# Kernel optimization log

Hardware: AMD Instinct MI355X
Metric: run time of the kernel (lower is better)

Reference implementation:

```python
import jax, jax.numpy as jnp
import numpy as np

B, G, NPA, NT, L = 8192, 689, 16, 131, 6
S = G + NPA * NT  # 2785 = 689 genes + 16 nodes per each of 131 assemblies


def setup_inputs() -> dict:
    key = jax.random.key(0)
    ks = jax.random.split(key, 8)
    x = jax.random.normal(ks[0], (B, G), dtype=jnp.float32)
    # depth-0 mask: place the 689 gene inputs into the first 689 slots of the layer
    lm0 = jnp.zeros((G, S), jnp.float32).at[jnp.arange(G), jnp.arange(G)].set(1.0)
    # per-depth sparse binary connectivity masks (ontology DAG edges at each depth)
    lm = (jax.random.uniform(ks[1], (L, S, S)) < 0.02).astype(jnp.float32)
    # diagonal pass-through masks for edges skipping this depth (stored as diagonals)
    flm_diag = (jax.random.uniform(ks[2], (L, S)) < 0.3).astype(jnp.float32)
    # final assembly selector: the nodes_per_assembly slots of the root assembly
    fasm = jnp.zeros((S,), jnp.float32).at[G:G + NPA].set(1.0)
    W0 = jax.random.normal(ks[3], (G, S), dtype=jnp.float32) * 0.05
    b0 = jnp.zeros((S,), jnp.float32)
    W = jax.random.normal(ks[4], (L, S, S), dtype=jnp.float32) * 0.05
    b = jnp.zeros((L, S), jnp.float32)
    gamma = jnp.ones((L + 1, S), jnp.float32)
    beta = jnp.zeros((L + 1, S), jnp.float32)
    w_out = jax.random.normal(ks[5], (S,), dtype=jnp.float32) * 0.05
    b_out = jnp.zeros((), jnp.float32)
    return {"x": x, "lm0": lm0, "lm": lm, "flm_diag": flm_diag, "fasm": fasm,
            "W0": W0, "b0": b0, "W": W, "b": b, "gamma": gamma, "beta": beta,
            "w_out": w_out, "b_out": b_out}


def _bn(h, g, bt, eps=1e-5):
    # training-mode BatchNorm1d over the batch axis
    m = h.mean(axis=0)
    v = h.var(axis=0)
    return (h - m) * jax.lax.rsqrt(v + eps) * g + bt


def reference(x, lm0, lm, flm_diag, fasm, W0, b0, W, b, gamma, beta, w_out, b_out):
    # depth 0: masked linear placing genes into layer slots, BN before activation
    h = jnp.tanh(_bn(x @ (W0 * lm0) + b0, gamma[0], beta[0]))  # [B, S]
    def step(h, layer):
        Wl, bl, lml, dl, gl, btl = layer
        # masked linear + BN + activation, plus diagonal pass-through skip
        hn = jnp.tanh(_bn(h @ (Wl * lml) + bl, gl, btl)) + h * dl
        return hn, None
    h, _ = jax.lax.scan(step, h, (W, b, lm, flm_diag, gamma[1:], beta[1:]))
    # output_method='final': linear head on final-assembly nodes only
    return (h * fasm) @ w_out + b_out  # [B]
```

## Files before the change

### kernel.cpp

```cpp
#include <hip/hip_runtime.h>
#include <hip/hip_fp16.h>
#include <stdint.h>

typedef uint32_t u32;
typedef uint64_t u64;
typedef unsigned int v4u __attribute__((ext_vector_type(4)));
typedef float v4f __attribute__((ext_vector_type(4)));
typedef _Float16 v2h __attribute__((ext_vector_type(2)));

constexpr int CB   = 8192;
constexpr int CG   = 689;
constexpr int CL   = 6;
constexpr int CS   = 2785;
constexpr int CSP  = 2816;
constexpr int CRS  = 8256;
constexpr int KCAP = 112;

union V16 { v4u u; v2h h2[4]; };
union F4  { v4f v; float f[4]; u32 u[4]; };
union HW  { u32 u; v2h h; };

__global__ __launch_bounds__(256) void build_main(const float* __restrict__ lm,
                                                  const float* __restrict__ W,
                                                  u64* __restrict__ ent,
                                                  int* __restrict__ cnt)
{
    int rb = blockIdx.x;
    int l  = rb / CS;
    int j  = rb - l * CS;
    const float* lrow = lm + (size_t)rb * CS;
    const float* wrow = W  + (size_t)rb * CS;
    u64 hi = ((u64)((u32)j * (u32)(CRS * 2))) << 32;
    int colbase = l * CSP;

    for (int s4 = threadIdx.x * 4; s4 < CS; s4 += 1024) {
        if (s4 + 4 <= CS) {
            F4 m4; m4.v = *reinterpret_cast<const v4f*>(lrow + s4);
            if ((m4.u[0] | m4.u[1] | m4.u[2] | m4.u[3]) == 0u) continue;
            F4 w4; w4.v = *reinterpret_cast<const v4f*>(wrow + s4);
#pragma unroll
            for (int q = 0; q < 4; q++) {
                if (m4.f[q] != 0.0f) {
                    int s = s4 + q;
                    int pos = atomicAdd(&cnt[colbase + s], 1);
                    if (pos < KCAP) {
                        u32 hw = (u32)__half_as_ushort(__float2half(w4.f[q]));
                        ent[(size_t)(colbase + s) * KCAP + pos] = hi | (u64)(hw | (hw << 16));
                    }
                }
            }
        } else {
            for (int s = s4; s < CS; s++) {
                float m = lrow[s];
                if (m != 0.0f) {
                    int pos = atomicAdd(&cnt[colbase + s], 1);
                    if (pos < KCAP) {
                        u32 hw = (u32)__half_as_ushort(__float2half(wrow[s]));
                        ent[(size_t)(colbase + s) * KCAP + pos] = hi | (u64)(hw | (hw << 16));
                    }
                }
            }
        }
    }
}

__global__ __launch_bounds__(256) void build0(const float* __restrict__ lm0,
                                              const float* __restrict__ W0,
                                              u64* __restrict__ ent,
                                              int* __restrict__ cnt)
{
    int j = blockIdx.x;
    const float* lrow = lm0 + (size_t)j * CS;
    const float* wrow = W0  + (size_t)j * CS;
    u64 hi = ((u64)((u32)j * (u32)(CRS * 2))) << 32;
    for (int s4 = threadIdx.x * 4; s4 < CS; s4 += 1024) {
        if (s4 + 4 <= CS) {
            F4 m4; m4.v = *reinterpret_cast<const v4f*>(lrow + s4);
            if ((m4.u[0] | m4.u[1] | m4.u[2] | m4.u[3]) == 0u) continue;
            F4 w4; w4.v = *reinterpret_cast<const v4f*>(wrow + s4);
#pragma unroll
            for (int q = 0; q < 4; q++) {
                if (m4.f[q] != 0.0f) {
                    int s = s4 + q;
                    int pos = atomicAdd(&cnt[s], 1);
                    if (pos < KCAP) {
                        u32 hw = (u32)__half_as_ushort(__float2half(w4.f[q]));
                        ent[(size_t)s * KCAP + pos] = hi | (u64)(hw | (hw << 16));
                    }
                }
            }
        } else {
            for (int s = s4; s < CS; s++) {
                float m = lrow[s];
                if (m != 0.0f) {
                    int pos = atomicAdd(&cnt[s], 1);
                    if (pos < KCAP) {
                        u32 hw = (u32)__half_as_ushort(__float2half(wrow[s]));
                        ent[(size_t)s * KCAP + pos] = hi | (u64)(hw | (hw << 16));
                    }
                }
            }
        }
    }
}

__global__ __launch_bounds__(256) void transpose_x(const float* __restrict__ x,
                                                   __half* __restrict__ xT)
{
    __shared__ float tile[32][33];
    int gx = blockIdx.x * 32;
    int gy = blockIdx.y * 32;
    int tx = threadIdx.x, ty = threadIdx.y;
#pragma unroll
    for (int i = 0; i < 32; i += 8) {
        int g = gx + tx;
        int b = gy + ty + i;
        tile[ty + i][tx] = (g < CG) ? x[(size_t)b * CG + g] : 0.f;
    }
    __syncthreads();
#pragma unroll
    for (int i = 0; i < 32; i += 8) {
        int g = gx + ty + i;
        int b = gy + tx;
        if (g < CG) xT[(size_t)g * CRS + b] = __float2half(tile[tx][ty + i]);
    }
}

__global__ __launch_bounds__(64) void gather_k(const __half* __restrict__ src,
                                               __half* __restrict__ dst,
                                               const u64* __restrict__ ent,
                                               const int* __restrict__ cnt,
                                               const float* __restrict__ bias,
                                               float* __restrict__ sumv,
                                               float* __restrict__ sumq,
                                               const int* __restrict__ sel,
                                               const int* __restrict__ selcnt)
{
    int s;
    if (sel) {
        if ((int)blockIdx.y >= *selcnt) return;
        s = sel[blockIdx.y];
    } else {
        s = blockIdx.y;
    }
    int lane = threadIdx.x;
    int boff = blockIdx.z * 4096 + blockIdx.x * 512 + lane * 8;

    int n = cnt[s]; if (n > KCAP) n = KCAP;
    int ng = (n + 7) >> 3;
    const u64* e = ent + (size_t)s * KCAP;
    const char* sb = (const char*)src + (size_t)boff * 2;

    float bv = bias[s];
    float acc[8];
#pragma unroll
    for (int j = 0; j < 8; j++) acc[j] = bv;

    for (int g = 0; g < ng; g++) {
        u64 ev[8];
#pragma unroll
        for (int q = 0; q < 8; q++) ev[q] = e[g * 8 + q];
        V16 rv[8];
#pragma unroll
        for (int q = 0; q < 8; q++)
            rv[q].u = *reinterpret_cast<const v4u*>(sb + (u32)(ev[q] >> 32));
#pragma unroll
        for (int q = 0; q < 8; q++) {
            HW w2; w2.u = (u32)ev[q];
#pragma unroll
            for (int j = 0; j < 4; j++) {
                float2 a2;
                a2.x = acc[2*j]; a2.y = acc[2*j+1];
#if __has_builtin(__builtin_amdgcn_fdot2)
#endif
                (void)a2;
                float2 f = __half22float2(*(const __half2*)&rv[q].h2[j]);
                float w = __half2float(*(const __half*)&w2.h);
                acc[2*j]   = fmaf(w, f.x, acc[2*j]);
                acc[2*j+1] = fmaf(w, f.y, acc[2*j+1]);
            }
        }
    }

    V16 o;
#pragma unroll
    for (int j = 0; j < 4; j++) {
        v2h p; p.x = (_Float16)acc[2*j]; p.y = (_Float16)acc[2*j+1];
        o.h2[j] = p;
    }
    __builtin_nontemporal_store(o.u, reinterpret_cast<v4u*>(dst + (size_t)s * CRS + boff));

    float ls = 0.f, lq = 0.f;
#pragma unroll
    for (int j = 0; j < 8; j++) { ls += acc[j]; lq += acc[j] * acc[j]; }
#pragma unroll
    for (int off = 32; off > 0; off >>= 1) {
        ls += __shfl_xor(ls, off);
        lq += __shfl_xor(lq, off);
    }
    if (lane == 0) { atomicAdd(&sumv[s], ls); atomicAdd(&sumq[s], lq); }
}

__global__ __launch_bounds__(64) void bn_act(__half* __restrict__ h,
                                             const __half* __restrict__ prev,
                                             const float* __restrict__ sumv,
                                             const float* __restrict__ sumq,
                                             const float* __restrict__ gamma,
                                             const float* __restrict__ beta,
                                             const float* __restrict__ dlv)
{
    int s = blockIdx.y;
    int boff = blockIdx.x * 512 + threadIdx.x * 8;
    float mean = sumv[s] * (1.0f / CB);
    float var  = sumq[s] * (1.0f / CB) - mean * mean;
    float rstd = rsqrtf(var + 1e-5f);
    float scale = gamma[s] * rstd;
    float shift = beta[s] - mean * scale;
    size_t base = (size_t)s * CRS + boff;
    V16 v; v.u = *reinterpret_cast<const v4u*>(h + base);
    V16 pv;
    float d = 0.f;
    if (prev) { d = dlv[s]; pv.u = *reinterpret_cast<const v4u*>(prev + base); }
    V16 o;
#pragma unroll
    for (int j = 0; j < 4; j++) {
        float2 f = __half22float2(*(const __half2*)&v.h2[j]);
        float t0 = tanhf(fmaf(f.x, scale, shift));
        float t1 = tanhf(fmaf(f.y, scale, shift));
        if (prev) {
            float2 p = __half22float2(*(const __half2*)&pv.h2[j]);
            t0 = fmaf(d, p.x, t0);
            t1 = fmaf(d, p.y, t1);
        }
        v2h pk; pk.x = (_Float16)t0; pk.y = (_Float16)t1;
        o.h2[j] = pk;
    }
    *reinterpret_cast<v4u*>(h + base) = o.u;
}

__global__ __launch_bounds__(256) void head_prep(const float* __restrict__ fasm,
                                                 const float* __restrict__ wout,
                                                 int* __restrict__ hcnt,
                                                 int* __restrict__ hs,
                                                 float* __restrict__ hc)
{
    int s = blockIdx.x * 256 + threadIdx.x;
    if (s >= CS) return;
    float c = fasm[s] * wout[s];
    if (c != 0.f) {
        int p = atomicAdd(hcnt, 1);
        if (p < 64) { hs[p] = s; hc[p] = c; }
    }
}

__global__ __launch_bounds__(256) void head_k(const __half* __restrict__ h6pre,
                                              const __half* __restrict__ h5,
                                              const int* __restrict__ hcnt,
                                              const int* __restrict__ hs,
                                              const float* __restrict__ hc,
                                              const float* __restrict__ sumv,
                                              const float* __restrict__ sumq,
                                              const float* __restrict__ gamma,
                                              const float* __restrict__ beta,
                                              const float* __restrict__ dlv,
                                              const float* __restrict__ bout,
                                              float* __restrict__ out)
{
    int b = blockIdx.x * 256 + threadIdx.x;
    int n = *hcnt; if (n > 64) n = 64;
    float acc = bout[0];
    for (int k = 0; k < n; k++) {
        int s = hs[k];
        float mean = sumv[s] * (1.0f / CB);
        float var  = sumq[s] * (1.0f / CB) - mean * mean;
        float rstd = rsqrtf(var + 1e-5f);
        float scale = gamma[s] * rstd;
        float shift = beta[s] - mean * scale;
        float pre  = __half2float(h6pre[(size_t)s * CRS + b]);
        float prev = __half2float(h5[(size_t)s * CRS + b]);
        float hn = tanhf(fmaf(pre, scale, shift)) + dlv[s] * prev;
        acc = fmaf(hc[k], hn, acc);
    }
    out[b] = acc;
}

extern "C" void kernel_launch(void* const* d_in, const int* in_sizes, int n_in,
                              void* d_out, int out_size, void* d_ws, size_t ws_size,
                              hipStream_t stream)
{
    const float* x    = (const float*)d_in[0];
    const float* lm0  = (const float*)d_in[1];
    const float* lm   = (const float*)d_in[2];
    const float* flm  = (const float*)d_in[3];
    const float* fasm = (const float*)d_in[4];
    const float* W0   = (const float*)d_in[5];
    const float* b0   = (const float*)d_in[6];
    const float* W    = (const float*)d_in[7];
    const float* bb   = (const float*)d_in[8];
    const float* gam  = (const float*)d_in[9];
    const float* bet  = (const float*)d_in[10];
    const float* wout = (const float*)d_in[11];
    const float* bout = (const float*)d_in[12];
    float* out = (float*)d_out;

    char* ws = (char*)d_ws;
    int*    cnt  = (int*)ws;
    float*  sumv = (float*)(ws + 78848);
    float*  sumq = (float*)(ws + 157696);
    int*    hcnt = (int*)(ws + 236544);
    int*    hs   = (int*)(ws + 236560);
    float*  hc   = (float*)(ws + 236816);
    u64*    ent  = (u64*)(ws + 237184);
    __half* hA   = (__half*)(ws + 17899136);
    __half* hB   = (__half*)(ws + 63885056);
    __half* xT   = hB;

    (void)hipMemsetAsync(ws, 0, 17899136, stream);

    build_main<<<dim3(CL * CS), 256, 0, stream>>>(lm, W, ent + (size_t)CSP * KCAP, cnt + CSP);
    build0    <<<dim3(CG),      256, 0, stream>>>(lm0, W0, ent, cnt);
    transpose_x<<<dim3(22, 256), dim3(32, 8), 0, stream>>>(x, xT);
    head_prep<<<dim3(11), 256, 0, stream>>>(fasm, wout, hcnt, hs, hc);

    const __half* cur = xT;
    __half* bufs[2] = {hA, hB};
    int which = 0;
    for (int t = 0; t < 6; t++) {
        __half* dst = bufs[which];
        const float* bias = (t == 0) ? b0 : bb + (size_t)(t - 1) * CS;
        gather_k<<<dim3(8, CS, 2), 64, 0, stream>>>(cur, dst,
            ent + (size_t)t * CSP * KCAP, cnt + t * CSP, bias,
            sumv + t * CSP, sumq + t * CSP, nullptr, nullptr);
        bn_act<<<dim3(16, CS), 64, 0, stream>>>(dst, (t == 0) ? nullptr : cur,
            sumv + t * CSP, sumq + t * CSP, gam + (size_t)t * CS, bet + (size_t)t * CS,
            (t == 0) ? nullptr : flm + (size_t)(t - 1) * CS);
        cur = dst;
        which ^= 1;
    }
    __half* h6 = bufs[which];
    gather_k<<<dim3(8, 16, 2), 64, 0, stream>>>(cur, h6,
        ent + (size_t)6 * CSP * KCAP, cnt + 6 * CSP, bb + (size_t)5 * CS,
        sumv + 6 * CSP, sumq + 6 * CSP, hs, hcnt);
    head_k<<<dim3(32), 256, 0, stream>>>(h6, cur, hcnt, hs, hc,
        sumv + 6 * CSP, sumq + 6 * CSP, gam + (size_t)6 * CS, bet + (size_t)6 * CS,
        flm + (size_t)5 * CS, bout, out);
}
```

Measured before the change: 1.197 ms.

## Build sparse CSC via per-row CSR slab, shrink memset, tidy gather tail

```diff
diff --git a/kernel.cpp b/kernel.cpp
--- a/kernel.cpp
+++ b/kernel.cpp
@@ -6,7 +6,6 @@
 typedef uint64_t u64;
 typedef unsigned int v4u __attribute__((ext_vector_type(4)));
 typedef float v4f __attribute__((ext_vector_type(4)));
-typedef _Float16 v2h __attribute__((ext_vector_type(2)));
 
 constexpr int CB   = 8192;
 constexpr int CG   = 689;
@@ -15,23 +14,24 @@
 constexpr int CSP  = 2816;
 constexpr int CRS  = 8256;
 constexpr int KCAP = 112;
-
-union V16 { v4u u; v2h h2[4]; };
+constexpr int RCAP = 112;
+
+union V16 { v4u u; _Float16 h[8]; };
 union F4  { v4f v; float f[4]; u32 u[4]; };
-union HW  { u32 u; v2h h; };
-
-__global__ __launch_bounds__(256) void build_main(const float* __restrict__ lm,
-                                                  const float* __restrict__ W,
-                                                  u64* __restrict__ ent,
-                                                  int* __restrict__ cnt)
+union HW  { u32 u; _Float16 h[2]; };
+
+__global__ __launch_bounds__(256) void build_csr(const float* __restrict__ lm,
+                                                 const float* __restrict__ W,
+                                                 u32* __restrict__ slab,
+                                                 int* __restrict__ rcnt)
 {
     int rb = blockIdx.x;
-    int l  = rb / CS;
-    int j  = rb - l * CS;
     const float* lrow = lm + (size_t)rb * CS;
     const float* wrow = W  + (size_t)rb * CS;
-    u64 hi = ((u64)((u32)j * (u32)(CRS * 2))) << 32;
-    int colbase = l * CSP;
+    u32* out = slab + (size_t)rb * RCAP;
+    __shared__ int lc;
+    if (threadIdx.x == 0) lc = 0;
+    __syncthreads();
 
     for (int s4 = threadIdx.x * 4; s4 < CS; s4 += 1024) {
         if (s4 + 4 <= CS) {
@@ -41,26 +41,48 @@
 #pragma unroll
             for (int q = 0; q < 4; q++) {
                 if (m4.f[q] != 0.0f) {
-                    int s = s4 + q;
-                    int pos = atomicAdd(&cnt[colbase + s], 1);
-                    if (pos < KCAP) {
+                    int pos = atomicAdd(&lc, 1);
+                    if (pos < RCAP) {
                         u32 hw = (u32)__half_as_ushort(__float2half(w4.f[q]));
-                        ent[(size_t)(colbase + s) * KCAP + pos] = hi | (u64)(hw | (hw << 16));
+                        out[pos] = ((u32)(s4 + q) << 16) | hw;
                     }
                 }
             }
         } else {
             for (int s = s4; s < CS; s++) {
-                float m = lrow[s];
-                if (m != 0.0f) {
-                    int pos = atomicAdd(&cnt[colbase + s], 1);
-                    if (pos < KCAP) {
+                if (lrow[s] != 0.0f) {
+                    int pos = atomicAdd(&lc, 1);
+                    if (pos < RCAP) {
                         u32 hw = (u32)__half_as_ushort(__float2half(wrow[s]));
-                        ent[(size_t)(colbase + s) * KCAP + pos] = hi | (u64)(hw | (hw << 16));
+                        out[pos] = ((u32)s << 16) | hw;
                     }
                 }
             }
         }
+    }
+    __syncthreads();
+    if (threadIdx.x == 0) rcnt[rb] = (lc < RCAP) ? lc : RCAP;
+}
+
+__global__ __launch_bounds__(256) void build_csc(const u32* __restrict__ slab,
+                                                 const int* __restrict__ rcnt,
+                                                 u64* __restrict__ ent,
+                                                 int* __restrict__ cnt)
+{
+    int i = blockIdx.x * 256 + threadIdx.x;
+    if (i >= CL * CS * RCAP) return;
+    int row = i / RCAP;
+    int pos = i - row * RCAP;
+    if (pos >= rcnt[row]) return;
+    u32 e = slab[i];
+    int l = row / CS;
+    int j = row - l * CS;
+    u32 hw = e & 0xffffu;
+    int col = l * CSP + (int)(e >> 16);
+    int p = atomicAdd(&cnt[col], 1);
+    if (p < KCAP) {
+        u64 hi = ((u64)((u32)j * (u32)(CRS * 2))) << 32;
+        ent[(size_t)col * KCAP + p] = hi | (u64)(hw | (hw << 16));
     }
 }
 
@@ -73,32 +95,12 @@
     const float* lrow = lm0 + (size_t)j * CS;
     const float* wrow = W0  + (size_t)j * CS;
     u64 hi = ((u64)((u32)j * (u32)(CRS * 2))) << 32;
-    for (int s4 = threadIdx.x * 4; s4 < CS; s4 += 1024) {
-        if (s4 + 4 <= CS) {
-            F4 m4; m4.v = *reinterpret_cast<const v4f*>(lrow + s4);
-            if ((m4.u[0] | m4.u[1] | m4.u[2] | m4.u[3]) == 0u) continue;
-            F4 w4; w4.v = *reinterpret_cast<const v4f*>(wrow + s4);
-#pragma unroll
-            for (int q = 0; q < 4; q++) {
-                if (m4.f[q] != 0.0f) {
-                    int s = s4 + q;
-                    int pos = atomicAdd(&cnt[s], 1);
-                    if (pos < KCAP) {
-                        u32 hw = (u32)__half_as_ushort(__float2half(w4.f[q]));
-                        ent[(size_t)s * KCAP + pos] = hi | (u64)(hw | (hw << 16));
-                    }
-                }
-            }
-        } else {
-            for (int s = s4; s < CS; s++) {
-                float m = lrow[s];
-                if (m != 0.0f) {
-                    int pos = atomicAdd(&cnt[s], 1);
-                    if (pos < KCAP) {
-                        u32 hw = (u32)__half_as_ushort(__float2half(wrow[s]));
-                        ent[(size_t)s * KCAP + pos] = hi | (u64)(hw | (hw << 16));
-                    }
-                }
+    for (int s = threadIdx.x; s < CS; s += 256) {
+        if (lrow[s] != 0.0f) {
+            int pos = atomicAdd(&cnt[s], 1);
+            if (pos < KCAP) {
+                u32 hw = (u32)__half_as_ushort(__float2half(wrow[s]));
+                ent[(size_t)s * KCAP + pos] = hi | (u64)(hw | (hw << 16));
             }
         }
     }
@@ -147,7 +149,8 @@
     int boff = blockIdx.z * 4096 + blockIdx.x * 512 + lane * 8;
 
     int n = cnt[s]; if (n > KCAP) n = KCAP;
-    int ng = (n + 7) >> 3;
+    int ngf = n >> 3;
+    int rem = n & 7;
     const u64* e = ent + (size_t)s * KCAP;
     const char* sb = (const char*)src + (size_t)boff * 2;
 
@@ -156,7 +159,7 @@
 #pragma unroll
     for (int j = 0; j < 8; j++) acc[j] = bv;
 
-    for (int g = 0; g < ng; g++) {
+    for (int g = 0; g < ngf; g++) {
         u64 ev[8];
 #pragma unroll
         for (int q = 0; q < 8; q++) ev[q] = e[g * 8 + q];
@@ -167,27 +170,36 @@
 #pragma unroll
         for (int q = 0; q < 8; q++) {
             HW w2; w2.u = (u32)ev[q];
-#pragma unroll
-            for (int j = 0; j < 4; j++) {
-                float2 a2;
-                a2.x = acc[2*j]; a2.y = acc[2*j+1];
-#if __has_builtin(__builtin_amdgcn_fdot2)
-#endif
-                (void)a2;
-                float2 f = __half22float2(*(const __half2*)&rv[q].h2[j]);
-                float w = __half2float(*(const __half*)&w2.h);
-                acc[2*j]   = fmaf(w, f.x, acc[2*j]);
-                acc[2*j+1] = fmaf(w, f.y, acc[2*j+1]);
-            }
+            float wf = (float)w2.h[0];
+#pragma unroll
+            for (int j = 0; j < 8; j++)
+                acc[j] = fmaf(wf, (float)rv[q].h[j], acc[j]);
+        }
+    }
+    if (rem) {
+        int base = ngf * 8;
+        u64 ev[8];
+#pragma unroll
+        for (int q = 0; q < 8; q++) ev[q] = e[base + q];
+        V16 rv[8];
+#pragma unroll
+        for (int q = 0; q < 8; q++) {
+            u32 off = (q < rem) ? (u32)(ev[q] >> 32) : 0u;
+            rv[q].u = *reinterpret_cast<const v4u*>(sb + off);
+        }
+#pragma unroll
+        for (int q = 0; q < 8; q++) {
+            HW w2; w2.u = (u32)ev[q];
+            float wf = (q < rem) ? (float)w2.h[0] : 0.f;
+#pragma unroll
+            for (int j = 0; j < 8; j++)
+                acc[j] = fmaf(wf, (float)rv[q].h[j], acc[j]);
         }
     }
 
     V16 o;
 #pragma unroll
-    for (int j = 0; j < 4; j++) {
-        v2h p; p.x = (_Float16)acc[2*j]; p.y = (_Float16)acc[2*j+1];
-        o.h2[j] = p;
-    }
+    for (int j = 0; j < 8; j++) o.h[j] = (_Float16)acc[j];
     __builtin_nontemporal_store(o.u, reinterpret_cast<v4u*>(dst + (size_t)s * CRS + boff));
 
     float ls = 0.f, lq = 0.f;
@@ -210,7 +222,7 @@
                                              const float* __restrict__ dlv)
 {
     int s = blockIdx.y;
-    int boff = blockIdx.x * 512 + threadIdx.x * 8;
+    int boff = (1 - (int)blockIdx.z) * 4096 + blockIdx.x * 512 + threadIdx.x * 8;
     float mean = sumv[s] * (1.0f / CB);
     float var  = sumq[s] * (1.0f / CB) - mean * mean;
     float rstd = rsqrtf(var + 1e-5f);
@@ -223,17 +235,10 @@
     if (prev) { d = dlv[s]; pv.u = *reinterpret_cast<const v4u*>(prev + base); }
     V16 o;
 #pragma unroll
-    for (int j = 0; j < 4; j++) {
-        float2 f = __half22float2(*(const __half2*)&v.h2[j]);
-        float t0 = tanhf(fmaf(f.x, scale, shift));
-        float t1 = tanhf(fmaf(f.y, scale, shift));
-        if (prev) {
-            float2 p = __half22float2(*(const __half2*)&pv.h2[j]);
-            t0 = fmaf(d, p.x, t0);
-            t1 = fmaf(d, p.y, t1);
-        }
-        v2h pk; pk.x = (_Float16)t0; pk.y = (_Float16)t1;
-        o.h2[j] = pk;
+    for (int j = 0; j < 8; j++) {
+        float t = tanhf(fmaf((float)v.h[j], scale, shift));
+        if (prev) t = fmaf(d, (float)pv.h[j], t);
+        o.h[j] = (_Float16)t;
     }
     *reinterpret_cast<v4u*>(h + base) = o.u;
 }
@@ -310,15 +315,19 @@
     int*    hcnt = (int*)(ws + 236544);
     int*    hs   = (int*)(ws + 236560);
     float*  hc   = (float*)(ws + 236816);
-    u64*    ent  = (u64*)(ws + 237184);
-    __half* hA   = (__half*)(ws + 17899136);
-    __half* hB   = (__half*)(ws + 63885056);
+    int*    rcnt = (int*)(ws + 237184);
+    u64*    ent  = (u64*)(ws + 304128);
+    __half* hA   = (__half*)(ws + 17966080);
+    __half* hB   = (__half*)(ws + 63952000);
+    u32*    slab = (u32*)hA;
     __half* xT   = hB;
 
-    (void)hipMemsetAsync(ws, 0, 17899136, stream);
-
-    build_main<<<dim3(CL * CS), 256, 0, stream>>>(lm, W, ent + (size_t)CSP * KCAP, cnt + CSP);
-    build0    <<<dim3(CG),      256, 0, stream>>>(lm0, W0, ent, cnt);
+    (void)hipMemsetAsync(ws, 0, 237184, stream);
+
+    build_csr<<<dim3(CL * CS), 256, 0, stream>>>(lm, W, slab, rcnt);
+    build_csc<<<dim3((CL * CS * RCAP + 255) / 256), 256, 0, stream>>>(slab, rcnt,
+        ent + (size_t)CSP * KCAP, cnt + CSP);
+    build0<<<dim3(CG), 256, 0, stream>>>(lm0, W0, ent, cnt);
     transpose_x<<<dim3(22, 256), dim3(32, 8), 0, stream>>>(x, xT);
     head_prep<<<dim3(11), 256, 0, stream>>>(fasm, wout, hcnt, hs, hc);
 
@@ -331,7 +340,7 @@
         gather_k<<<dim3(8, CS, 2), 64, 0, stream>>>(cur, dst,
             ent + (size_t)t * CSP * KCAP, cnt + t * CSP, bias,
             sumv + t * CSP, sumq + t * CSP, nullptr, nullptr);
-        bn_act<<<dim3(16, CS), 64, 0, stream>>>(dst, (t == 0) ? nullptr : cur,
+        bn_act<<<dim3(8, CS, 2), 64, 0, stream>>>(dst, (t == 0) ? nullptr : cur,
             sumv + t * CSP, sumq + t * CSP, gam + (size_t)t * CS, bet + (size_t)t * CS,
             (t == 0) ? nullptr : flm + (size_t)(t - 1) * CS);
         cur = dst;
```

After: 1.253 ms. 4.6% more time.
